# Optimization experiments

Hardware: AMD Instinct MI355X
Metric: run time of the kernel (lower is better)

## Reference

```python
import jax, jax.numpy as jnp
import numpy as np

# __init__ constants
COORS_RANGE = ((-51.2, 51.2), (-51.2, 51.2), (-4.0, 2.4))  # x, y, z ranges
SPATIAL = (512, 512, 64)  # base spatial shape (X, Y, Z)
SCALES = (2, 4, 8, 1)     # scale_list + [1]
N_POINTS = 2_000_000
N_BATCH = 8


def setup_inputs() -> dict:
    key = jax.random.key(0)
    kp, kb = jax.random.split(key)
    lo = jnp.array([r[0] for r in COORS_RANGE], dtype=jnp.float32)
    hi = jnp.array([r[1] for r in COORS_RANGE], dtype=jnp.float32)
    u = jax.random.uniform(kp, (N_POINTS, 3), dtype=jnp.float32)
    points = lo + u * (hi - lo)  # [N,3] xyz inside the voxelization range
    batch_idx = jax.random.randint(kb, (N_POINTS,), 0, N_BATCH).astype(jnp.int64)
    return {"points": points, "batch_idx": batch_idx}


def reference(points, batch_idx):
    """Per scale: quantize xyz to voxel indices, then unique/dedup with inverse and
    counts. Rows [b,x,y,z] are packed into a single int64 key so that a 1-D unique
    (lexicographically equivalent to torch.unique(dim=0)) can be used.
    Returns, for each scale in SCALES: (full_coors [N,4] int64, coors_inv [N] int,
    coors [M,4] int32 in [b,z,y,x] order), flattened into one tuple."""
    b = batch_idx.astype(jnp.int64)
    outs = []
    for scale in SCALES:
        dims = [int(np.ceil(s / scale)) for s in SPATIAL]  # per-scale grid size
        idxs = []
        for i in range(3):
            lo, hi = COORS_RANGE[i]
            # torch .long() truncates toward zero; values are >=0 in range so
            # truncation == floor here.
            idxs.append((dims[i] * (points[:, i] - lo) / (hi - lo)).astype(jnp.int64))
        xidx, yidx, zidx = idxs
        full_coors = jnp.stack([b, xidx, yidx, zidx], axis=-1)  # [N,4]
        sx, sy, sz = dims
        # pack (b,x,y,z) lexicographically into one key
        keys = ((b * sx + xidx) * sy + yidx) * sz + zidx
        unq, unq_inv, unq_cnt = jnp.unique(keys, return_inverse=True, return_counts=True)
        zb = unq % sz
        rem = unq // sz
        yb = rem % sy
        rem = rem // sy
        xb = rem % sx
        bb = rem // sx
        # original reorders unq columns to [b, z, y, x] and casts to int32
        coors = jnp.stack([bb, zb, yb, xb], axis=-1).astype(jnp.int32)
        outs.extend([full_coors, unq_inv.reshape(-1), coors])
    return tuple(outs)
```

## Files before the change

kernel.cpp:

```cpp
#include <hip/hip_runtime.h>
#include <stdint.h>


#define CHUNK 4096
#define NB    1174
#define TOTALW 4808704
#define R_S2 0
#define R_S4 528384
#define R_S8 598016
#define R_S1 610304
#define NBUCKET 512
#define BCAP 5120
#define KEYBLOCKS 1024
#define ROUND 2048
#define KPT 8

__device__ __forceinline__ uint32_t cmp2(uint32_t w) {
  w = (w | (w >> 1)) & 0x55555555u;
  w = (w | (w >> 1)) & 0x33333333u;
  w = (w | (w >> 2)) & 0x0F0F0F0Fu;
  w = (w | (w >> 4)) & 0x00FF00FFu;
  w = (w | (w >> 8)) & 0x0000FFFFu;
  return w;
}

__global__ __launch_bounds__(256) void k_key(
    const float* __restrict__ pts, const int* __restrict__ bidx, int n,
    uint32_t* __restrict__ keys, uint32_t* __restrict__ bitmap,
    uint32_t* __restrict__ bucketCount, uint32_t* __restrict__ bucketData) {
  __shared__ uint32_t cnt[NBUCKET], inc[NBUCKET], pos[NBUCKET], gpos[NBUCKET];
  __shared__ uint32_t shs[256];
  __shared__ uint32_t scratch[ROUND];
  int t = threadIdx.x;
  int base = blockIdx.x * ROUND;

  cnt[t] = 0; cnt[t + 256] = 0;
  pos[t] = 0; pos[t + 256] = 0;
  __syncthreads();

  uint32_t myKey[KPT];
  int myBk[KPT];
#pragma unroll
  for (int k = 0; k < KPT; k++) {
    int j = base + k * 256 + t;
    myBk[k] = -1;
    if (j < n) {
      float px = pts[3 * j + 0];
      float py = pts[3 * j + 1];
      float pz = pts[3 * j + 2];
      int b = bidx[j];
      int x1 = (int)((512.0f * (px + 51.2f)) / 102.4f);
      int y1 = (int)((512.0f * (py + 51.2f)) / 102.4f);
      int z1 = (int)((64.0f * (pz + 4.0f)) / 6.4f);
      keys[j] = ((uint32_t)b << 27) | ((uint32_t)x1 << 17) | ((uint32_t)y1 << 7) | (uint32_t)z1;
      uint32_t s1k = (uint32_t)(((b * 512 + x1) * 512 + y1) * 64 + z1);
      if (s1k >= (1u << 27)) {
        atomicOr(&bitmap[R_S1 + (s1k >> 5)], 1u << (s1k & 31u));
        uint32_t k2 = (uint32_t)(((b * 256 + (x1 >> 1)) * 256 + (y1 >> 1)) * 32 + (z1 >> 1));
        atomicOr(&bitmap[R_S2 + (k2 >> 5)], 1u << (k2 & 31u));
        uint32_t k4 = (uint32_t)(((b * 128 + (x1 >> 2)) * 128 + (y1 >> 2)) * 16 + (z1 >> 2));
        atomicOr(&bitmap[R_S4 + (k4 >> 5)], 1u << (k4 & 31u));
        uint32_t k8 = (uint32_t)(((b * 64 + (x1 >> 3)) * 64 + (y1 >> 3)) * 8 + (z1 >> 3));
        atomicOr(&bitmap[R_S8 + (k8 >> 5)], 1u << (k8 & 31u));
      } else {
        int bk = (int)(s1k >> 18);
        myBk[k] = bk;
        myKey[k] = s1k;
        atomicAdd(&cnt[bk], 1u);
      }
    }
  }
  __syncthreads();

  uint32_t c0 = cnt[2 * t], c1 = cnt[2 * t + 1];
  gpos[2 * t] = c0 ? atomicAdd(&bucketCount[2 * t], c0) : 0u;
  gpos[2 * t + 1] = c1 ? atomicAdd(&bucketCount[2 * t + 1], c1) : 0u;
  uint32_t s = c0 + c1;
  shs[t] = s;
  __syncthreads();
  for (int off = 1; off < 256; off <<= 1) {
    uint32_t add = (t >= off) ? shs[t - off] : 0u;
    __syncthreads();
    shs[t] += add;
    __syncthreads();
  }
  inc[2 * t] = shs[t] - s + c0;
  inc[2 * t + 1] = shs[t];
  __syncthreads();
  uint32_t total = shs[255];

#pragma unroll
  for (int k = 0; k < KPT; k++) {
    if (myBk[k] >= 0) {
      int bk = myBk[k];
      uint32_t slot = inc[bk] - cnt[bk] + atomicAdd(&pos[bk], 1u);
      scratch[slot] = myKey[k];
    }
  }
  __syncthreads();

#pragma unroll
  for (int m = 0; m < KPT; m++) {
    uint32_t p = (uint32_t)(m * 256 + t);
    if (p < total) {
      int lo = 0, hi = NBUCKET - 1;
      while (lo < hi) {
        int mid = (lo + hi) >> 1;
        if (inc[mid] > p) hi = mid; else lo = mid + 1;
      }
      uint32_t lidx = p - (inc[lo] - cnt[lo]);
      uint32_t g = gpos[lo] + lidx;
      if (g < BCAP) bucketData[(size_t)lo * BCAP + g] = scratch[p];
    }
  }
}

__global__ __launch_bounds__(256) void k_bucket(
    const uint32_t* __restrict__ bucketCount, const uint32_t* __restrict__ bucketData,
    uint32_t* __restrict__ bitmap) {
  __shared__ uint32_t s1L[8192];
  __shared__ uint32_t s2L[1024];
  __shared__ uint32_t s4L[128];
  int bk = blockIdx.x, t = threadIdx.x;

  uint4 z4 = make_uint4(0, 0, 0, 0);
  for (int i = t; i < 2048; i += 256) ((uint4*)s1L)[i] = z4;
  __syncthreads();

  uint32_t c = bucketCount[bk];
  if (c > BCAP) c = BCAP;
  const uint32_t* src = bucketData + (size_t)bk * BCAP;
  for (uint32_t i = t; i < c; i += 256) {
    uint32_t key = src[i];
    uint32_t local = key & 0x3FFFFu;
    atomicOr(&s1L[local >> 5], 1u << (local & 31u));
  }
  __syncthreads();

  uint4* g1 = (uint4*)(bitmap + R_S1 + (size_t)bk * 8192);
  for (int i = t; i < 2048; i += 256) g1[i] = ((uint4*)s1L)[i];

  for (int i = t; i < 1024; i += 256) {
    int x2r = i >> 8, Y2 = i & 255;
    int a = (2 * x2r * 512 + 2 * Y2) * 2;
    int b2 = ((2 * x2r + 1) * 512 + 2 * Y2) * 2;
    uint32_t Ax = s1L[a], Ay = s1L[a + 1], Az = s1L[a + 2], Aw = s1L[a + 3];
    uint32_t Bx = s1L[b2], By = s1L[b2 + 1], Bz = s1L[b2 + 2], Bw = s1L[b2 + 3];
    s2L[i] = cmp2(Ax | Az | Bx | Bz) | (cmp2(Ay | Aw | By | Bw) << 16);
  }
  __syncthreads();
  for (int i = t; i < 1024; i += 256) bitmap[R_S2 + (size_t)bk * 1024 + i] = s2L[i];

  if (t < 128) {
    int x4r = t >> 6, kk = t & 63;
    int a = (2 * x4r) * 256 + 4 * kk;
    int b4 = (2 * x4r + 1) * 256 + 4 * kk;
    uint32_t A0 = s2L[a], A1 = s2L[a + 1], A2 = s2L[a + 2], A3 = s2L[a + 3];
    uint32_t B0 = s2L[b4], B1 = s2L[b4 + 1], B2 = s2L[b4 + 2], B3 = s2L[b4 + 3];
    s4L[t] = cmp2(A0 | A1 | B0 | B1) | (cmp2(A2 | A3 | B2 | B3) << 16);
  }
  __syncthreads();
  if (t < 128) bitmap[R_S4 + (size_t)bk * 128 + t] = s4L[t];

  if (t < 16) {
    uint32_t res = 0;
#pragma unroll
    for (int j = 0; j < 4; j++) {
      uint32_t u = s4L[4 * t + j] | s4L[64 + 4 * t + j];
      u = (u | (u >> 16)) & 0xFFFFu;
      res |= cmp2(u) << (8 * j);
    }
    bitmap[R_S8 + (size_t)bk * 16 + t] = res;
  }
}

__global__ __launch_bounds__(256) void k_sumA(
    const uint32_t* __restrict__ bitmap, uint32_t* __restrict__ blockSums) {
  __shared__ uint32_t sh[256];
  int t = threadIdx.x;
  const uint4* bp = (const uint4*)(bitmap + (size_t)blockIdx.x * CHUNK + t * 16);
  uint32_t s = 0;
#pragma unroll
  for (int k = 0; k < 4; k++) {
    uint4 v = bp[k];
    s += __popc(v.x) + __popc(v.y) + __popc(v.z) + __popc(v.w);
  }
  sh[t] = s;
  __syncthreads();
  for (int off = 128; off > 0; off >>= 1) {
    if (t < off) sh[t] += sh[t + off];
    __syncthreads();
  }
  if (t == 0) blockSums[blockIdx.x] = sh[0];
}

__global__ __launch_bounds__(256) void k_scanB(
    uint32_t* blockSums, long long* devOff, uint32_t* devRank, long long fiveN) {
  __shared__ uint32_t sh[256];
  __shared__ uint32_t shB[3];
  int t = threadIdx.x;
  uint32_t v[8];
  uint32_t s = 0;
#pragma unroll
  for (int k = 0; k < 8; k++) {
    int idx = t * 8 + k;
    uint32_t x = (idx < NB) ? blockSums[idx] : 0u;
    v[k] = x;
    s += x;
  }
  sh[t] = s;
  __syncthreads();
  for (int off = 1; off < 256; off <<= 1) {
    uint32_t add = (t >= off) ? sh[t - off] : 0u;
    __syncthreads();
    sh[t] += add;
    __syncthreads();
  }
  uint32_t run = sh[t] - s;
#pragma unroll
  for (int k = 0; k < 8; k++) {
    int idx = t * 8 + k;
    if (idx < NB) blockSums[idx] = run;
    if (idx == 129) shB[0] = run;
    if (idx == 146) shB[1] = run;
    if (idx == 149) shB[2] = run;
    run += v[k];
  }
  __syncthreads();
  if (t == 0) {
    uint32_t tot = sh[255];
    uint32_t T0 = shB[0];
    uint32_t T1 = shB[1] - shB[0];
    uint32_t T2 = shB[2] - shB[1];
    uint32_t T3 = tot - shB[2];
    devOff[0] = 0;
    devOff[1] = devOff[0] + fiveN + 4LL * T0;
    devOff[2] = devOff[1] + fiveN + 4LL * T1;
    devOff[3] = devOff[2] + fiveN + 4LL * T2;
    devOff[4] = devOff[3] + fiveN + 4LL * T3;
    devRank[0] = 0;
    devRank[1] = shB[0];
    devRank[2] = shB[1];
    devRank[3] = shB[2];
  }
}

__global__ __launch_bounds__(256) void k_pref(
    const uint32_t* __restrict__ bitmap, const uint32_t* __restrict__ blockSums,
    uint2* __restrict__ pairs) {
  __shared__ uint32_t sh[256];
  int t = threadIdx.x;
  size_t w0 = (size_t)blockIdx.x * CHUNK + t * 16;
  const uint4* bp = (const uint4*)(bitmap + w0);
  uint4 words[4];
  uint32_t s = 0;
#pragma unroll
  for (int k = 0; k < 4; k++) {
    uint4 v = bp[k];
    words[k] = v;
    s += __popc(v.x) + __popc(v.y) + __popc(v.z) + __popc(v.w);
  }
  sh[t] = s;
  __syncthreads();
  for (int off = 1; off < 256; off <<= 1) {
    uint32_t add = (t >= off) ? sh[t - off] : 0u;
    __syncthreads();
    sh[t] += add;
    __syncthreads();
  }
  uint32_t run = blockSums[blockIdx.x] + (sh[t] - s);
  uint4* pp = (uint4*)(pairs + w0);
#pragma unroll
  for (int k = 0; k < 4; k++) {
    uint4 o1, o2;
    o1.x = words[k].x; o1.y = run; run += __popc(words[k].x);
    o1.z = words[k].y; o1.w = run; run += __popc(words[k].y);
    o2.x = words[k].z; o2.y = run; run += __popc(words[k].z);
    o2.z = words[k].w; o2.w = run; run += __popc(words[k].w);
    pp[2 * k] = o1;
    pp[2 * k + 1] = o2;
  }
}

__global__ __launch_bounds__(256) void k_write(
    const uint32_t* __restrict__ keys, int n, const uint2* __restrict__ pairs,
    const uint32_t* __restrict__ devRank, const long long* __restrict__ devOff,
    int* __restrict__ out, long long fourN) {
  int j = blockIdx.x * 256 + threadIdx.x;
  if (j >= n) return;
  uint32_t p = keys[j];
  int b = (int)(p >> 27);
  int x1 = (int)((p >> 17) & 1023u);
  int y1 = (int)((p >> 7) & 1023u);
  int z1 = (int)(p & 127u);
  const int SX[4] = {256, 128, 64, 512};
  const int SY[4] = {256, 128, 64, 512};
  const int SZ[4] = {32, 16, 8, 64};
  const int SH[4] = {1, 2, 3, 0};
  const int RG[4] = {R_S2, R_S4, R_S8, R_S1};
#pragma unroll
  for (int i = 0; i < 4; i++) {
    int sh = SH[i];
    int xi = x1 >> sh, yi = y1 >> sh, zi = z1 >> sh;
    uint32_t key = (uint32_t)(((b * SX[i] + xi) * SY[i] + yi) * SZ[i] + zi);
    uint2 pr = pairs[RG[i] + (key >> 5)];
    long long o = devOff[i];
    *(int4*)(out + o + 4LL * j) = make_int4(b, xi, yi, zi);
    uint32_t inv = pr.y + __popc(pr.x & ((1u << (key & 31u)) - 1u)) - devRank[i];
    out[o + fourN + j] = (int)inv;
  }
}

template <int LZ, int LYZ, int LB, int MZ, int MY, int MX, int RG, int SCALE_IDX>
__device__ __forceinline__ void uniq_region(
    uint32_t w, uint32_t wd, uint32_t pf, uint32_t rankBase,
    const long long* __restrict__ devOff, int* __restrict__ out, long long fiveN) {
  uint32_t pos = pf - rankBase;
  long long base = devOff[SCALE_IDX] + fiveN;
  uint32_t local = w - (uint32_t)RG;
  while (wd) {
    int bit = __ffs(wd) - 1;
    wd &= wd - 1u;
    uint32_t key = (local << 5) + (uint32_t)bit;
    int z = (int)(key & (uint32_t)MZ);
    int y = (int)((key >> LZ) & (uint32_t)MY);
    int x = (int)((key >> LYZ) & (uint32_t)MX);
    int bb = (int)(key >> LB);
    *(int4*)(out + base + 4LL * pos) = make_int4(bb, z, y, x);
    pos++;
  }
}

__global__ __launch_bounds__(256) void k_uniq(
    const uint2* __restrict__ pairs, const uint32_t* __restrict__ devRank,
    const long long* __restrict__ devOff, int* __restrict__ out, long long fiveN) {
  uint32_t w = blockIdx.x * 256 + threadIdx.x;
  uint2 pr = pairs[w];
  if (!pr.x) return;
  if (w < R_S4) {
    uniq_region<5, 13, 21, 31, 255, 255, R_S2, 0>(w, pr.x, pr.y, devRank[0], devOff, out, fiveN);
  } else if (w < R_S8) {
    uniq_region<4, 11, 18, 15, 127, 127, R_S4, 1>(w, pr.x, pr.y, devRank[1], devOff, out, fiveN);
  } else if (w < R_S1) {
    uniq_region<3, 9, 15, 7, 63, 63, R_S8, 2>(w, pr.x, pr.y, devRank[2], devOff, out, fiveN);
  } else {
    uniq_region<6, 15, 24, 63, 511, 511, R_S1, 3>(w, pr.x, pr.y, devRank[3], devOff, out, fiveN);
  }
}

extern "C" void kernel_launch(void* const* d_in, const int* in_sizes, int n_in,
                              void* d_out, int out_size, void* d_ws, size_t ws_size,
                              hipStream_t stream) {
  const float* pts = (const float*)d_in[0];
  const int* bidx = (const int*)d_in[1];
  int n = in_sizes[0] / 3;
  int* out = (int*)d_out;

  char* ws = (char*)d_ws;
  long long* devOff = (long long*)ws;
  uint32_t* devRank = (uint32_t*)(ws + 64);
  uint32_t* chunkSums = (uint32_t*)(ws + 256);
  uint32_t* bucketCount = (uint32_t*)(ws + 5120);
  uint32_t* bitmap = (uint32_t*)(ws + 8192);
  uint2* pairs = (uint2*)(ws + 19243008);
  uint32_t* keys = (uint32_t*)(ws + 57712640);
  uint32_t* bucketData = (uint32_t*)(ws + 65712640);

  const long long fourN = 4LL * n, fiveN = 5LL * n;
  const int gridN = (n + 255) / 256;

  hipMemsetAsync(bitmap, 0, (size_t)TOTALW * 4, stream);
  hipMemsetAsync(bucketCount, 0, NBUCKET * 4, stream);
  hipLaunchKernelGGL(k_key, dim3(KEYBLOCKS), dim3(256), 0, stream,
                     pts, bidx, n, keys, bitmap, bucketCount, bucketData);
  hipLaunchKernelGGL(k_bucket, dim3(NBUCKET), dim3(256), 0, stream,
                     bucketCount, bucketData, bitmap);
  hipLaunchKernelGGL(k_sumA, dim3(NB), dim3(256), 0, stream, bitmap, chunkSums);
  hipLaunchKernelGGL(k_scanB, dim3(1), dim3(256), 0, stream, chunkSums, devOff, devRank, fiveN);
  hipLaunchKernelGGL(k_pref, dim3(NB), dim3(256), 0, stream, bitmap, chunkSums, pairs);
  hipLaunchKernelGGL(k_write, dim3(gridN), dim3(256), 0, stream,
                     keys, n, pairs, devRank, devOff, out, fourN);
  hipLaunchKernelGGL(k_uniq, dim3(TOTALW / 256), dim3(256), 0, stream,
                     pairs, devRank, devOff, out, fiveN);
}
```

Before: 449.2 us.

## Fuse prefix-scan with unique-coordinate decode and drop bucket binary search

Merges the bitmap prefix kernel and the unique-decode kernel into one launch. Each block now decodes set bits straight from registers right after computing the running rank, so the pairs array no longer has to be re-read for decoding. The scatter stage takes the bucket id from the key's high bits instead of binary-searching the inclusive counts. k_write now handles two points per thread with half as many blocks. Block-range boundaries are hardcoded to map chunks to scales, which adds a dependence on the region layout and more divergence inside decode.

```diff
diff --git a/kernel.cpp b/kernel.cpp
--- a/kernel.cpp
+++ b/kernel.cpp
@@ -103,14 +103,11 @@
   for (int m = 0; m < KPT; m++) {
     uint32_t p = (uint32_t)(m * 256 + t);
     if (p < total) {
-      int lo = 0, hi = NBUCKET - 1;
-      while (lo < hi) {
-        int mid = (lo + hi) >> 1;
-        if (inc[mid] > p) hi = mid; else lo = mid + 1;
-      }
+      uint32_t kk = scratch[p];
+      int lo = (int)(kk >> 18);
       uint32_t lidx = p - (inc[lo] - cnt[lo]);
       uint32_t g = gpos[lo] + lidx;
-      if (g < BCAP) bucketData[(size_t)lo * BCAP + g] = scratch[p];
+      if (g < BCAP) bucketData[(size_t)lo * BCAP + g] = kk;
     }
   }
 }
@@ -245,74 +242,8 @@
   }
 }
 
-__global__ __launch_bounds__(256) void k_pref(
-    const uint32_t* __restrict__ bitmap, const uint32_t* __restrict__ blockSums,
-    uint2* __restrict__ pairs) {
-  __shared__ uint32_t sh[256];
-  int t = threadIdx.x;
-  size_t w0 = (size_t)blockIdx.x * CHUNK + t * 16;
-  const uint4* bp = (const uint4*)(bitmap + w0);
-  uint4 words[4];
-  uint32_t s = 0;
-#pragma unroll
-  for (int k = 0; k < 4; k++) {
-    uint4 v = bp[k];
-    words[k] = v;
-    s += __popc(v.x) + __popc(v.y) + __popc(v.z) + __popc(v.w);
-  }
-  sh[t] = s;
-  __syncthreads();
-  for (int off = 1; off < 256; off <<= 1) {
-    uint32_t add = (t >= off) ? sh[t - off] : 0u;
-    __syncthreads();
-    sh[t] += add;
-    __syncthreads();
-  }
-  uint32_t run = blockSums[blockIdx.x] + (sh[t] - s);
-  uint4* pp = (uint4*)(pairs + w0);
-#pragma unroll
-  for (int k = 0; k < 4; k++) {
-    uint4 o1, o2;
-    o1.x = words[k].x; o1.y = run; run += __popc(words[k].x);
-    o1.z = words[k].y; o1.w = run; run += __popc(words[k].y);
-    o2.x = words[k].z; o2.y = run; run += __popc(words[k].z);
-    o2.z = words[k].w; o2.w = run; run += __popc(words[k].w);
-    pp[2 * k] = o1;
-    pp[2 * k + 1] = o2;
-  }
-}
-
-__global__ __launch_bounds__(256) void k_write(
-    const uint32_t* __restrict__ keys, int n, const uint2* __restrict__ pairs,
-    const uint32_t* __restrict__ devRank, const long long* __restrict__ devOff,
-    int* __restrict__ out, long long fourN) {
-  int j = blockIdx.x * 256 + threadIdx.x;
-  if (j >= n) return;
-  uint32_t p = keys[j];
-  int b = (int)(p >> 27);
-  int x1 = (int)((p >> 17) & 1023u);
-  int y1 = (int)((p >> 7) & 1023u);
-  int z1 = (int)(p & 127u);
-  const int SX[4] = {256, 128, 64, 512};
-  const int SY[4] = {256, 128, 64, 512};
-  const int SZ[4] = {32, 16, 8, 64};
-  const int SH[4] = {1, 2, 3, 0};
-  const int RG[4] = {R_S2, R_S4, R_S8, R_S1};
-#pragma unroll
-  for (int i = 0; i < 4; i++) {
-    int sh = SH[i];
-    int xi = x1 >> sh, yi = y1 >> sh, zi = z1 >> sh;
-    uint32_t key = (uint32_t)(((b * SX[i] + xi) * SY[i] + yi) * SZ[i] + zi);
-    uint2 pr = pairs[RG[i] + (key >> 5)];
-    long long o = devOff[i];
-    *(int4*)(out + o + 4LL * j) = make_int4(b, xi, yi, zi);
-    uint32_t inv = pr.y + __popc(pr.x & ((1u << (key & 31u)) - 1u)) - devRank[i];
-    out[o + fourN + j] = (int)inv;
-  }
-}
-
 template <int LZ, int LYZ, int LB, int MZ, int MY, int MX, int RG, int SCALE_IDX>
-__device__ __forceinline__ void uniq_region(
+__device__ __forceinline__ void decode_word(
     uint32_t w, uint32_t wd, uint32_t pf, uint32_t rankBase,
     const long long* __restrict__ devOff, int* __restrict__ out, long long fiveN) {
   uint32_t pos = pf - rankBase;
@@ -331,20 +262,103 @@
   }
 }
 
-__global__ __launch_bounds__(256) void k_uniq(
-    const uint2* __restrict__ pairs, const uint32_t* __restrict__ devRank,
+template <int LZ, int LYZ, int LB, int MZ, int MY, int MX, int RG, int SCALE_IDX>
+__device__ __forceinline__ void pref_uniq_body(
+    const uint32_t* __restrict__ bitmap, const uint32_t* __restrict__ blockSums,
+    uint2* __restrict__ pairs, const uint32_t* __restrict__ devRank,
     const long long* __restrict__ devOff, int* __restrict__ out, long long fiveN) {
-  uint32_t w = blockIdx.x * 256 + threadIdx.x;
-  uint2 pr = pairs[w];
-  if (!pr.x) return;
-  if (w < R_S4) {
-    uniq_region<5, 13, 21, 31, 255, 255, R_S2, 0>(w, pr.x, pr.y, devRank[0], devOff, out, fiveN);
-  } else if (w < R_S8) {
-    uniq_region<4, 11, 18, 15, 127, 127, R_S4, 1>(w, pr.x, pr.y, devRank[1], devOff, out, fiveN);
-  } else if (w < R_S1) {
-    uniq_region<3, 9, 15, 7, 63, 63, R_S8, 2>(w, pr.x, pr.y, devRank[2], devOff, out, fiveN);
+  __shared__ uint32_t sh[256];
+  int t = threadIdx.x;
+  size_t w0 = (size_t)blockIdx.x * CHUNK + t * 16;
+  const uint4* bp = (const uint4*)(bitmap + w0);
+  uint4 words[4];
+  uint32_t s = 0;
+#pragma unroll
+  for (int k = 0; k < 4; k++) {
+    uint4 v = bp[k];
+    words[k] = v;
+    s += __popc(v.x) + __popc(v.y) + __popc(v.z) + __popc(v.w);
+  }
+  sh[t] = s;
+  __syncthreads();
+  for (int off = 1; off < 256; off <<= 1) {
+    uint32_t add = (t >= off) ? sh[t - off] : 0u;
+    __syncthreads();
+    sh[t] += add;
+    __syncthreads();
+  }
+  uint32_t run = blockSums[blockIdx.x] + (sh[t] - s);
+  uint32_t rankBase = devRank[SCALE_IDX];
+  uint4* pp = (uint4*)(pairs + w0);
+#pragma unroll
+  for (int k = 0; k < 4; k++) {
+    uint4 o1, o2;
+    uint32_t wa = words[k].x, wb = words[k].y, wc = words[k].z, wdd = words[k].w;
+    o1.x = wa; o1.y = run;
+    if (wa) decode_word<LZ, LYZ, LB, MZ, MY, MX, RG, SCALE_IDX>(
+        (uint32_t)(w0 + 4 * k + 0), wa, run, rankBase, devOff, out, fiveN);
+    run += __popc(wa);
+    o1.z = wb; o1.w = run;
+    if (wb) decode_word<LZ, LYZ, LB, MZ, MY, MX, RG, SCALE_IDX>(
+        (uint32_t)(w0 + 4 * k + 1), wb, run, rankBase, devOff, out, fiveN);
+    run += __popc(wb);
+    o2.x = wc; o2.y = run;
+    if (wc) decode_word<LZ, LYZ, LB, MZ, MY, MX, RG, SCALE_IDX>(
+        (uint32_t)(w0 + 4 * k + 2), wc, run, rankBase, devOff, out, fiveN);
+    run += __popc(wc);
+    o2.z = wdd; o2.w = run;
+    if (wdd) decode_word<LZ, LYZ, LB, MZ, MY, MX, RG, SCALE_IDX>(
+        (uint32_t)(w0 + 4 * k + 3), wdd, run, rankBase, devOff, out, fiveN);
+    run += __popc(wdd);
+    pp[2 * k] = o1;
+    pp[2 * k + 1] = o2;
+  }
+}
+
+__global__ __launch_bounds__(256) void k_pref_uniq(
+    const uint32_t* __restrict__ bitmap, const uint32_t* __restrict__ blockSums,
+    uint2* __restrict__ pairs, const uint32_t* __restrict__ devRank,
+    const long long* __restrict__ devOff, int* __restrict__ out, long long fiveN) {
+  if (blockIdx.x < 129) {
+    pref_uniq_body<5, 13, 21, 31, 255, 255, R_S2, 0>(bitmap, blockSums, pairs, devRank, devOff, out, fiveN);
+  } else if (blockIdx.x < 146) {
+    pref_uniq_body<4, 11, 18, 15, 127, 127, R_S4, 1>(bitmap, blockSums, pairs, devRank, devOff, out, fiveN);
+  } else if (blockIdx.x < 149) {
+    pref_uniq_body<3, 9, 15, 7, 63, 63, R_S8, 2>(bitmap, blockSums, pairs, devRank, devOff, out, fiveN);
   } else {
-    uniq_region<6, 15, 24, 63, 511, 511, R_S1, 3>(w, pr.x, pr.y, devRank[3], devOff, out, fiveN);
+    pref_uniq_body<6, 15, 24, 63, 511, 511, R_S1, 3>(bitmap, blockSums, pairs, devRank, devOff, out, fiveN);
+  }
+}
+
+__global__ __launch_bounds__(256) void k_write(
+    const uint32_t* __restrict__ keys, int n, const uint2* __restrict__ pairs,
+    const uint32_t* __restrict__ devRank, const long long* __restrict__ devOff,
+    int* __restrict__ out, long long fourN) {
+  const int SX[4] = {256, 128, 64, 512};
+  const int SY[4] = {256, 128, 64, 512};
+  const int SZ[4] = {32, 16, 8, 64};
+  const int SH[4] = {1, 2, 3, 0};
+  const int RG[4] = {R_S2, R_S4, R_S8, R_S1};
+#pragma unroll
+  for (int half = 0; half < 2; half++) {
+    int j = blockIdx.x * 512 + half * 256 + threadIdx.x;
+    if (j >= n) continue;
+    uint32_t p = keys[j];
+    int b = (int)(p >> 27);
+    int x1 = (int)((p >> 17) & 1023u);
+    int y1 = (int)((p >> 7) & 1023u);
+    int z1 = (int)(p & 127u);
+#pragma unroll
+    for (int i = 0; i < 4; i++) {
+      int sh = SH[i];
+      int xi = x1 >> sh, yi = y1 >> sh, zi = z1 >> sh;
+      uint32_t key = (uint32_t)(((b * SX[i] + xi) * SY[i] + yi) * SZ[i] + zi);
+      uint2 pr = pairs[RG[i] + (key >> 5)];
+      long long o = devOff[i];
+      *(int4*)(out + o + 4LL * j) = make_int4(b, xi, yi, zi);
+      uint32_t inv = pr.y + __popc(pr.x & ((1u << (key & 31u)) - 1u)) - devRank[i];
+      out[o + fourN + j] = (int)inv;
+    }
   }
 }
 
@@ -367,7 +381,7 @@
   uint32_t* bucketData = (uint32_t*)(ws + 65712640);
 
   const long long fourN = 4LL * n, fiveN = 5LL * n;
-  const int gridN = (n + 255) / 256;
+  const int gridW = (n + 511) / 512;
 
   hipMemsetAsync(bitmap, 0, (size_t)TOTALW * 4, stream);
   hipMemsetAsync(bucketCount, 0, NBUCKET * 4, stream);
@@ -377,9 +391,8 @@
                      bucketCount, bucketData, bitmap);
   hipLaunchKernelGGL(k_sumA, dim3(NB), dim3(256), 0, stream, bitmap, chunkSums);
   hipLaunchKernelGGL(k_scanB, dim3(1), dim3(256), 0, stream, chunkSums, devOff, devRank, fiveN);
-  hipLaunchKernelGGL(k_pref, dim3(NB), dim3(256), 0, stream, bitmap, chunkSums, pairs);
-  hipLaunchKernelGGL(k_write, dim3(gridN), dim3(256), 0, stream,
+  hipLaunchKernelGGL(k_pref_uniq, dim3(NB), dim3(256), 0, stream,
+                     bitmap, chunkSums, pairs, devRank, devOff, out, fiveN);
+  hipLaunchKernelGGL(k_write, dim3(gridW), dim3(256), 0, stream,
                      keys, n, pairs, devRank, devOff, out, fourN);
-  hipLaunchKernelGGL(k_uniq, dim3(TOTALW / 256), dim3(256), 0, stream,
-                     pairs, devRank, devOff, out, fiveN);
-}
+}
```

Result: slower. 518.5 us (+15.4%).

## Fuse popcount chunk sums into bucket kernel and drop full bitmap memset

Applied to the files above, without the earlier changes.

The separate k_sumA popcount pass is removed. k_bucket now computes per-chunk popcounts for each scale while writing the bitmaps, reduces them in shared memory, and writes or atomically adds them into chunkSums. The 19 MB bitmap memset is replaced by zeroing only the pad regions plus a small chunkSums memset. The fallback path for keys with batch index 8 or higher is dropped, and the bucket lookup in k_key now takes the bucket from the key instead of a binary search. k_write also handles two points per thread with hoisted offsets, at the cost of several block reductions and relying on every bitmap word being covered by a bucket.

```diff
diff --git a/kernel.cpp b/kernel.cpp
--- a/kernel.cpp
+++ b/kernel.cpp
@@ -9,6 +9,10 @@
 #define R_S4 528384
 #define R_S8 598016
 #define R_S1 610304
+#define PAD0 524288
+#define PAD1 593920
+#define PAD2 606208
+#define PAD3 4804608
 #define NBUCKET 512
 #define BCAP 5120
 #define KEYBLOCKS 1024
@@ -26,7 +30,7 @@
 
 __global__ __launch_bounds__(256) void k_key(
     const float* __restrict__ pts, const int* __restrict__ bidx, int n,
-    uint32_t* __restrict__ keys, uint32_t* __restrict__ bitmap,
+    uint32_t* __restrict__ keys,
     uint32_t* __restrict__ bucketCount, uint32_t* __restrict__ bucketData) {
   __shared__ uint32_t cnt[NBUCKET], inc[NBUCKET], pos[NBUCKET], gpos[NBUCKET];
   __shared__ uint32_t shs[256];
@@ -54,15 +58,7 @@
       int z1 = (int)((64.0f * (pz + 4.0f)) / 6.4f);
       keys[j] = ((uint32_t)b << 27) | ((uint32_t)x1 << 17) | ((uint32_t)y1 << 7) | (uint32_t)z1;
       uint32_t s1k = (uint32_t)(((b * 512 + x1) * 512 + y1) * 64 + z1);
-      if (s1k >= (1u << 27)) {
-        atomicOr(&bitmap[R_S1 + (s1k >> 5)], 1u << (s1k & 31u));
-        uint32_t k2 = (uint32_t)(((b * 256 + (x1 >> 1)) * 256 + (y1 >> 1)) * 32 + (z1 >> 1));
-        atomicOr(&bitmap[R_S2 + (k2 >> 5)], 1u << (k2 & 31u));
-        uint32_t k4 = (uint32_t)(((b * 128 + (x1 >> 2)) * 128 + (y1 >> 2)) * 16 + (z1 >> 2));
-        atomicOr(&bitmap[R_S4 + (k4 >> 5)], 1u << (k4 & 31u));
-        uint32_t k8 = (uint32_t)(((b * 64 + (x1 >> 3)) * 64 + (y1 >> 3)) * 8 + (z1 >> 3));
-        atomicOr(&bitmap[R_S8 + (k8 >> 5)], 1u << (k8 & 31u));
-      } else {
+      if (s1k < (1u << 27)) {
         int bk = (int)(s1k >> 18);
         myBk[k] = bk;
         myKey[k] = s1k;
@@ -103,28 +99,44 @@
   for (int m = 0; m < KPT; m++) {
     uint32_t p = (uint32_t)(m * 256 + t);
     if (p < total) {
-      int lo = 0, hi = NBUCKET - 1;
-      while (lo < hi) {
-        int mid = (lo + hi) >> 1;
-        if (inc[mid] > p) hi = mid; else lo = mid + 1;
-      }
+      uint32_t kk = scratch[p];
+      int lo = (int)(kk >> 18);
       uint32_t lidx = p - (inc[lo] - cnt[lo]);
       uint32_t g = gpos[lo] + lidx;
-      if (g < BCAP) bucketData[(size_t)lo * BCAP + g] = scratch[p];
+      if (g < BCAP) bucketData[(size_t)lo * BCAP + g] = kk;
     }
   }
+}
+
+__device__ __forceinline__ uint32_t blockReduce(uint32_t v, uint32_t* shR, int t) {
+  shR[t] = v;
+  __syncthreads();
+  for (int off = 128; off > 0; off >>= 1) {
+    if (t < off) shR[t] += shR[t + off];
+    __syncthreads();
+  }
+  uint32_t r = shR[0];
+  __syncthreads();
+  return r;
 }
 
 __global__ __launch_bounds__(256) void k_bucket(
     const uint32_t* __restrict__ bucketCount, const uint32_t* __restrict__ bucketData,
-    uint32_t* __restrict__ bitmap) {
+    uint32_t* __restrict__ bitmap, uint32_t* __restrict__ chunkSums) {
   __shared__ uint32_t s1L[8192];
   __shared__ uint32_t s2L[1024];
   __shared__ uint32_t s4L[128];
+  __shared__ uint32_t shR[256];
   int bk = blockIdx.x, t = threadIdx.x;
 
   uint4 z4 = make_uint4(0, 0, 0, 0);
   for (int i = t; i < 2048; i += 256) ((uint4*)s1L)[i] = z4;
+
+  if (bk < 4) {
+    const int pads[4] = {PAD0, PAD1, PAD2, PAD3};
+    uint4* pz = (uint4*)(bitmap + pads[bk]);
+    for (int i = t; i < 1024; i += 256) pz[i] = z4;
+  }
   __syncthreads();
 
   uint32_t c = bucketCount[bk];
@@ -138,7 +150,13 @@
   __syncthreads();
 
   uint4* g1 = (uint4*)(bitmap + R_S1 + (size_t)bk * 8192);
-  for (int i = t; i < 2048; i += 256) g1[i] = ((uint4*)s1L)[i];
+  uint32_t pc1a = 0, pc1b = 0;
+  for (int i = t; i < 2048; i += 256) {
+    uint4 v = ((uint4*)s1L)[i];
+    g1[i] = v;
+    uint32_t pc = __popc(v.x) + __popc(v.y) + __popc(v.z) + __popc(v.w);
+    if (i < 1024) pc1a += pc; else pc1b += pc;
+  }
 
   for (int i = t; i < 1024; i += 256) {
     int x2r = i >> 8, Y2 = i & 255;
@@ -149,19 +167,28 @@
     s2L[i] = cmp2(Ax | Az | Bx | Bz) | (cmp2(Ay | Aw | By | Bw) << 16);
   }
   __syncthreads();
-  for (int i = t; i < 1024; i += 256) bitmap[R_S2 + (size_t)bk * 1024 + i] = s2L[i];
-
+  uint32_t pc2 = 0;
+  for (int i = t; i < 1024; i += 256) {
+    uint32_t v = s2L[i];
+    bitmap[R_S2 + (size_t)bk * 1024 + i] = v;
+    pc2 += __popc(v);
+  }
+
+  uint32_t pc4 = 0;
   if (t < 128) {
     int x4r = t >> 6, kk = t & 63;
     int a = (2 * x4r) * 256 + 4 * kk;
     int b4 = (2 * x4r + 1) * 256 + 4 * kk;
     uint32_t A0 = s2L[a], A1 = s2L[a + 1], A2 = s2L[a + 2], A3 = s2L[a + 3];
     uint32_t B0 = s2L[b4], B1 = s2L[b4 + 1], B2 = s2L[b4 + 2], B3 = s2L[b4 + 3];
-    s4L[t] = cmp2(A0 | A1 | B0 | B1) | (cmp2(A2 | A3 | B2 | B3) << 16);
+    uint32_t v = cmp2(A0 | A1 | B0 | B1) | (cmp2(A2 | A3 | B2 | B3) << 16);
+    s4L[t] = v;
+    pc4 = __popc(v);
   }
   __syncthreads();
   if (t < 128) bitmap[R_S4 + (size_t)bk * 128 + t] = s4L[t];
 
+  uint32_t pc8 = 0;
   if (t < 16) {
     uint32_t res = 0;
 #pragma unroll
@@ -171,27 +198,21 @@
       res |= cmp2(u) << (8 * j);
     }
     bitmap[R_S8 + (size_t)bk * 16 + t] = res;
-  }
-}
-
-__global__ __launch_bounds__(256) void k_sumA(
-    const uint32_t* __restrict__ bitmap, uint32_t* __restrict__ blockSums) {
-  __shared__ uint32_t sh[256];
-  int t = threadIdx.x;
-  const uint4* bp = (const uint4*)(bitmap + (size_t)blockIdx.x * CHUNK + t * 16);
-  uint32_t s = 0;
-#pragma unroll
-  for (int k = 0; k < 4; k++) {
-    uint4 v = bp[k];
-    s += __popc(v.x) + __popc(v.y) + __popc(v.z) + __popc(v.w);
-  }
-  sh[t] = s;
-  __syncthreads();
-  for (int off = 128; off > 0; off >>= 1) {
-    if (t < off) sh[t] += sh[t + off];
-    __syncthreads();
-  }
-  if (t == 0) blockSums[blockIdx.x] = sh[0];
+    pc8 = __popc(res);
+  }
+
+  uint32_t S1a = blockReduce(pc1a, shR, t);
+  uint32_t S1b = blockReduce(pc1b, shR, t);
+  uint32_t S2 = blockReduce(pc2, shR, t);
+  uint32_t S4 = blockReduce(pc4, shR, t);
+  uint32_t S8 = blockReduce(pc8, shR, t);
+  if (t == 0) {
+    chunkSums[149 + 2 * bk] = S1a;
+    chunkSums[150 + 2 * bk] = S1b;
+    atomicAdd(&chunkSums[bk >> 2], S2);
+    atomicAdd(&chunkSums[129 + (bk >> 5)], S4);
+    atomicAdd(&chunkSums[146 + (bk >> 8)], S8);
+  }
 }
 
 __global__ __launch_bounds__(256) void k_scanB(
@@ -286,28 +307,35 @@
     const uint32_t* __restrict__ keys, int n, const uint2* __restrict__ pairs,
     const uint32_t* __restrict__ devRank, const long long* __restrict__ devOff,
     int* __restrict__ out, long long fourN) {
-  int j = blockIdx.x * 256 + threadIdx.x;
-  if (j >= n) return;
-  uint32_t p = keys[j];
-  int b = (int)(p >> 27);
-  int x1 = (int)((p >> 17) & 1023u);
-  int y1 = (int)((p >> 7) & 1023u);
-  int z1 = (int)(p & 127u);
   const int SX[4] = {256, 128, 64, 512};
   const int SY[4] = {256, 128, 64, 512};
   const int SZ[4] = {32, 16, 8, 64};
   const int SH[4] = {1, 2, 3, 0};
   const int RG[4] = {R_S2, R_S4, R_S8, R_S1};
-#pragma unroll
-  for (int i = 0; i < 4; i++) {
-    int sh = SH[i];
-    int xi = x1 >> sh, yi = y1 >> sh, zi = z1 >> sh;
-    uint32_t key = (uint32_t)(((b * SX[i] + xi) * SY[i] + yi) * SZ[i] + zi);
-    uint2 pr = pairs[RG[i] + (key >> 5)];
-    long long o = devOff[i];
-    *(int4*)(out + o + 4LL * j) = make_int4(b, xi, yi, zi);
-    uint32_t inv = pr.y + __popc(pr.x & ((1u << (key & 31u)) - 1u)) - devRank[i];
-    out[o + fourN + j] = (int)inv;
+  long long off[4];
+  uint32_t rnk[4];
+#pragma unroll
+  for (int i = 0; i < 4; i++) { off[i] = devOff[i]; rnk[i] = devRank[i]; }
+#pragma unroll
+  for (int half = 0; half < 2; half++) {
+    int j = blockIdx.x * 512 + half * 256 + threadIdx.x;
+    if (j >= n) continue;
+    uint32_t p = keys[j];
+    int b = (int)(p >> 27);
+    int x1 = (int)((p >> 17) & 1023u);
+    int y1 = (int)((p >> 7) & 1023u);
+    int z1 = (int)(p & 127u);
+#pragma unroll
+    for (int i = 0; i < 4; i++) {
+      int sh = SH[i];
+      int xi = x1 >> sh, yi = y1 >> sh, zi = z1 >> sh;
+      uint32_t key = (uint32_t)(((b * SX[i] + xi) * SY[i] + yi) * SZ[i] + zi);
+      uint2 pr = pairs[RG[i] + (key >> 5)];
+      long long o = off[i];
+      *(int4*)(out + o + 4LL * j) = make_int4(b, xi, yi, zi);
+      uint32_t inv = pr.y + __popc(pr.x & ((1u << (key & 31u)) - 1u)) - rnk[i];
+      out[o + fourN + j] = (int)inv;
+    }
   }
 }
 
@@ -367,18 +395,17 @@
   uint32_t* bucketData = (uint32_t*)(ws + 65712640);
 
   const long long fourN = 4LL * n, fiveN = 5LL * n;
-  const int gridN = (n + 255) / 256;
-
-  hipMemsetAsync(bitmap, 0, (size_t)TOTALW * 4, stream);
+  const int gridW = (n + 511) / 512;
+
+  hipMemsetAsync(chunkSums, 0, NB * 4, stream);
   hipMemsetAsync(bucketCount, 0, NBUCKET * 4, stream);
   hipLaunchKernelGGL(k_key, dim3(KEYBLOCKS), dim3(256), 0, stream,
-                     pts, bidx, n, keys, bitmap, bucketCount, bucketData);
+                     pts, bidx, n, keys, bucketCount, bucketData);
   hipLaunchKernelGGL(k_bucket, dim3(NBUCKET), dim3(256), 0, stream,
-                     bucketCount, bucketData, bitmap);
-  hipLaunchKernelGGL(k_sumA, dim3(NB), dim3(256), 0, stream, bitmap, chunkSums);
+                     bucketCount, bucketData, bitmap, chunkSums);
   hipLaunchKernelGGL(k_scanB, dim3(1), dim3(256), 0, stream, chunkSums, devOff, devRank, fiveN);
   hipLaunchKernelGGL(k_pref, dim3(NB), dim3(256), 0, stream, bitmap, chunkSums, pairs);
-  hipLaunchKernelGGL(k_write, dim3(gridN), dim3(256), 0, stream,
+  hipLaunchKernelGGL(k_write, dim3(gridW), dim3(256), 0, stream,
                      keys, n, pairs, devRank, devOff, out, fourN);
   hipLaunchKernelGGL(k_uniq, dim3(TOTALW / 256), dim3(256), 0, stream,
                      pairs, devRank, devOff, out, fiveN);
```

Result: no change. 449.4 us (+0.0%).
